# Kernel optimization log

Measured on AMD Instinct MI355X. Metric: run time of the kernel, lower is better.

The kernel has to match this reference:

```python
import jax, jax.numpy as jnp
import numpy as np

N = 100000          # nodes
E = 3200000         # directed edges
NUM_GRAPHS = 2000   # pooled segments
D = 64              # hidden dim
L = 3               # num_unit GCNConv layers


def setup_inputs() -> dict:
    key = jax.random.key(0)
    ks = jax.random.split(key, 12)
    x = jax.random.normal(ks[0], (N, 4), dtype=jnp.float32)
    edge_index = jax.random.randint(ks[1], (2, E), 0, N, dtype=jnp.int64)
    batch = jnp.sort(jax.random.randint(ks[2], (N,), 0, NUM_GRAPHS, dtype=jnp.int64))
    def lin(k, out_f, in_f):
        kw, kb = jax.random.split(k)
        lim = 1.0 / np.sqrt(in_f)
        W = jax.random.uniform(kw, (out_f, in_f), jnp.float32, -lim, lim)
        b = jax.random.uniform(kb, (out_f,), jnp.float32, -lim, lim)
        return W, b
    emb_w, emb_b = lin(ks[3], D, 4)
    cw, cb = [], []
    for i in range(L):
        W, b = lin(ks[4 + i], D, D)
        cw.append(W); cb.append(b)
    conv_w = jnp.stack(cw)   # [L, D, D]
    conv_b = jnp.stack(cb)   # [L, D]
    lin1_w, lin1_b = lin(ks[8], D, D)
    lin2_w, lin2_b = lin(ks[9], 3, D)
    return {"x": x, "edge_index": edge_index, "batch": batch,
            "emb_w": emb_w, "emb_b": emb_b, "conv_w": conv_w, "conv_b": conv_b,
            "lin1_w": lin1_w, "lin1_b": lin1_b, "lin2_w": lin2_w, "lin2_b": lin2_b}


def reference(x, edge_index, batch, emb_w, emb_b, conv_w, conv_b,
              lin1_w, lin1_b, lin2_w, lin2_b):
    # ---- GCN normalization (edge_weight = 1, self-loops added, shared across layers) ----
    loop = jnp.arange(N, dtype=edge_index.dtype)
    src = jnp.concatenate([edge_index[0], loop])   # [E+N]
    dst = jnp.concatenate([edge_index[1], loop])
    deg = jax.ops.segment_sum(jnp.ones_like(src, dtype=x.dtype), dst, num_segments=N)
    dinv = jnp.where(deg > 0, jax.lax.rsqrt(deg), 0.0)
    norm = dinv[src] * dinv[dst]                   # [E+N]

    # node embedding (dropout in eval mode = identity)
    h = x @ emb_w.T + emb_b                        # [N, D]

    # stacked GCNConv + ReLU: h' = scatter_add(norm * (h W^T)[src] -> dst) + b
    for l in range(L):
        t = h @ conv_w[l].T                        # [N, D]
        msg = t[src] * norm[:, None]               # gather + scale, [E+N, D]
        h = jax.ops.segment_sum(msg, dst, num_segments=N) + conv_b[l]
        h = jax.nn.relu(h)

    # global mean pool over graphs
    gsum = jax.ops.segment_sum(h, batch, num_segments=NUM_GRAPHS)        # [G, D]
    cnt = jax.ops.segment_sum(jnp.ones((N,), x.dtype), batch, num_segments=NUM_GRAPHS)
    gmean = gsum / jnp.maximum(cnt, 1.0)[:, None]

    # MLP head
    p = jax.nn.relu(gmean @ lin1_w.T + lin1_b)
    pred = p @ lin2_w.T + lin2_b                   # [G, 3]
    return pred
```

## Files before the change

kernel.cpp:

```cpp
#include <hip/hip_runtime.h>

__device__ __forceinline__ unsigned short f2bf(float f) {
    union { float f; unsigned int u; } c; c.f = f;
    unsigned int r = c.u + 0x7fffu + ((c.u >> 16) & 1u);
    return (unsigned short)(r >> 16);
}
__device__ __forceinline__ float bf2f(unsigned short b) {
    union { unsigned int u; float f; } c; c.u = ((unsigned int)b) << 16;
    return c.f;
}
__device__ __forceinline__ float bflo(unsigned int v) {
    union { unsigned int u; float f; } c; c.u = v << 16; return c.f;
}
__device__ __forceinline__ float bfhi(unsigned int v) {
    union { unsigned int u; float f; } c; c.u = v & 0xffff0000u; return c.f;
}


#define BIN_CAP 6144
#define MAX_BINS 1024

__global__ __launch_bounds__(256) void k_binA(const int* __restrict__ src,
                                              const int* __restrict__ dst,
                                              int* __restrict__ bincnt,
                                              int* __restrict__ binbuf,
                                              int E, int nbins) {
    __shared__ int hist[MAX_BINS];
    __shared__ int lbase[MAX_BINS];
    int tid = threadIdx.x;
    int chunk = (E + gridDim.x - 1) / gridDim.x;
    int e0 = blockIdx.x * chunk;
    int e1 = min(e0 + chunk, E);

    for (int i = tid; i < nbins; i += 256) hist[i] = 0;
    __syncthreads();
    for (int e = e0 + tid; e < e1; e += 256) atomicAdd(&hist[dst[e] >> 7], 1);
    __syncthreads();
    for (int i = tid; i < nbins; i += 256) {
        int c = hist[i];
        lbase[i] = c ? atomicAdd(&bincnt[i], c) : 0;
        hist[i] = 0;
    }
    __syncthreads();
    for (int e = e0 + tid; e < e1; e += 256) {
        int d = dst[e], s = src[e];
        int b = d >> 7;
        int pos = lbase[b] + atomicAdd(&hist[b], 1);
        binbuf[(size_t)b * BIN_CAP + pos] = ((d & 127) << 20) | s;
    }
}

__global__ void k_hist(const int* __restrict__ bincnt, const int* __restrict__ binbuf,
                       int* __restrict__ deg, float* __restrict__ dinv, int n) {
    __shared__ int h[128];
    int b = blockIdx.x, tid = threadIdx.x;
    if (tid < 128) h[tid] = 0;
    __syncthreads();
    int cnt = bincnt[b];
    const int* rec = binbuf + (size_t)b * BIN_CAP;
    for (int i = tid; i < cnt; i += 256) atomicAdd(&h[rec[i] >> 20], 1);
    __syncthreads();
    int node = b * 128 + tid;
    if (tid < 128 && node < n) {
        int d = h[tid];
        deg[node] = d;
        dinv[node] = rsqrtf((float)(d + 1));
    }
}

__global__ void k_scan1(const int* __restrict__ deg, int* __restrict__ rowptr,
                        int* __restrict__ bsum, int n) {
    __shared__ int s[256];
    int tid = threadIdx.x;
    int i = blockIdx.x * 256 + tid;
    int v = (i < n) ? deg[i] : 0;
    s[tid] = v;
    __syncthreads();
    for (int off = 1; off < 256; off <<= 1) {
        int t = (tid >= off) ? s[tid - off] : 0;
        __syncthreads();
        s[tid] += t;
        __syncthreads();
    }
    if (i < n) rowptr[i] = s[tid] - v;
    if (tid == 255) bsum[blockIdx.x] = s[255];
}

__global__ void k_scan2(int* __restrict__ bsum, int nb) {
    __shared__ int s[512];
    int tid = threadIdx.x;
    int v = (tid < nb) ? bsum[tid] : 0;
    s[tid] = v;
    __syncthreads();
    for (int off = 1; off < 512; off <<= 1) {
        int t = (tid >= off) ? s[tid - off] : 0;
        __syncthreads();
        s[tid] += t;
        __syncthreads();
    }
    if (tid < nb) bsum[tid] = s[tid] - v;
}

__global__ void k_scan3(int* __restrict__ rowptr, const int* __restrict__ bsum,
                        int n, int total) {
    int i = blockIdx.x * blockDim.x + threadIdx.x;
    if (i < n) rowptr[i] += bsum[i >> 8];
    if (i == 0) rowptr[n] = total;
}

__global__ void k_binB(const int* __restrict__ bincnt, const int* __restrict__ binbuf,
                       const int* __restrict__ rowptr, int* __restrict__ col, int n) {
    __shared__ int cur[128];
    int b = blockIdx.x, tid = threadIdx.x;
    int node = b * 128 + tid;
    if (tid < 128) cur[tid] = (node < n) ? rowptr[node] : 0;
    __syncthreads();
    int cnt = bincnt[b];
    const int* rec = binbuf + (size_t)b * BIN_CAP;
    for (int i = tid; i < cnt; i += 256) {
        int r = rec[i];
        int pos = atomicAdd(&cur[r >> 20], 1);
        col[pos] = r & ((1 << 20) - 1);
    }
}


__global__ __launch_bounds__(256) void k_gemm0(const float* __restrict__ x,
                                               const float* __restrict__ embw,
                                               const float* __restrict__ embb,
                                               const float* __restrict__ W,
                                               const float* __restrict__ dinv,
                                               unsigned short* __restrict__ uout, int n) {
    __shared__ float hN[64 * 68];
    __shared__ float wT[64 * 68];
    __shared__ float sX[64 * 4];
    __shared__ float sW[64 * 4];
    __shared__ float sB[64];
    int tid = threadIdx.x;
    int nbase = blockIdx.x * 64;
    for (int i = tid; i < 4096; i += 256) {
        int j = i >> 6, k = i & 63;
        wT[k * 68 + j] = W[i];
    }
    if (tid < 256) sW[tid] = embw[tid];
    if (tid < 64) sB[tid] = embb[tid];
    {
        int node = nbase + (tid >> 2);
        sX[tid] = (node < n) ? x[(size_t)node * 4 + (tid & 3)] : 0.f;
    }
    __syncthreads();
    for (int i = tid; i < 4096; i += 256) {
        int nn = i >> 6, k = i & 63;
        float s = sB[k];
        s = fmaf(sX[nn * 4 + 0], sW[k * 4 + 0], s);
        s = fmaf(sX[nn * 4 + 1], sW[k * 4 + 1], s);
        s = fmaf(sX[nn * 4 + 2], sW[k * 4 + 2], s);
        s = fmaf(sX[nn * 4 + 3], sW[k * 4 + 3], s);
        hN[nn * 68 + k] = s;
    }
    __syncthreads();

    int tx = tid & 15;
    int ty = tid >> 4;
    float acc[4][4] = {};
#pragma unroll
    for (int k0 = 0; k0 < 64; k0 += 4) {
        float a[4][4], w[4][4];
#pragma unroll
        for (int i = 0; i < 4; i++)
            *(float4*)a[i] = *(const float4*)&hN[(ty * 4 + i) * 68 + k0];
#pragma unroll
        for (int dk = 0; dk < 4; dk++)
            *(float4*)w[dk] = *(const float4*)&wT[(k0 + dk) * 68 + tx * 4];
#pragma unroll
        for (int i = 0; i < 4; i++)
#pragma unroll
            for (int j = 0; j < 4; j++)
#pragma unroll
                for (int dk = 0; dk < 4; dk++)
                    acc[i][j] = fmaf(a[i][dk], w[dk][j], acc[i][j]);
    }
#pragma unroll
    for (int i = 0; i < 4; i++) {
        int node = nbase + ty * 4 + i;
        if (node < n) {
            float sc = dinv[node];
            ushort4 o;
            o.x = f2bf(acc[i][0] * sc);
            o.y = f2bf(acc[i][1] * sc);
            o.z = f2bf(acc[i][2] * sc);
            o.w = f2bf(acc[i][3] * sc);
            *(ushort4*)&uout[(size_t)node * 64 + tx * 4] = o;
        }
    }
}

__global__ __launch_bounds__(256) void k_gemm(const unsigned short* __restrict__ hin,
                                              const float* __restrict__ W,
                                              const float* __restrict__ dinv,
                                              unsigned short* __restrict__ uout, int n) {
    __shared__ float hN[64 * 68];
    __shared__ float wT[64 * 68];
    int tid = threadIdx.x;
    int nbase = blockIdx.x * 64;
    for (int i = tid; i < 4096; i += 256) {
        int j = i >> 6, k = i & 63;
        wT[k * 68 + j] = W[i];
    }
    for (int i = tid; i < 2048; i += 256) {
        int nn = i >> 5, k2 = i & 31;
        int node = nbase + nn;
        unsigned int v = (node < n) ? ((const unsigned int*)hin)[(size_t)node * 32 + k2] : 0u;
        hN[nn * 68 + k2 * 2 + 0] = bflo(v);
        hN[nn * 68 + k2 * 2 + 1] = bfhi(v);
    }
    __syncthreads();

    int tx = tid & 15;
    int ty = tid >> 4;
    float acc[4][4] = {};
#pragma unroll
    for (int k0 = 0; k0 < 64; k0 += 4) {
        float a[4][4], w[4][4];
#pragma unroll
        for (int i = 0; i < 4; i++)
            *(float4*)a[i] = *(const float4*)&hN[(ty * 4 + i) * 68 + k0];
#pragma unroll
        for (int dk = 0; dk < 4; dk++)
            *(float4*)w[dk] = *(const float4*)&wT[(k0 + dk) * 68 + tx * 4];
#pragma unroll
        for (int i = 0; i < 4; i++)
#pragma unroll
            for (int j = 0; j < 4; j++)
#pragma unroll
                for (int dk = 0; dk < 4; dk++)
                    acc[i][j] = fmaf(a[i][dk], w[dk][j], acc[i][j]);
    }
#pragma unroll
    for (int i = 0; i < 4; i++) {
        int node = nbase + ty * 4 + i;
        if (node < n) {
            float sc = dinv[node];
            ushort4 o;
            o.x = f2bf(acc[i][0] * sc);
            o.y = f2bf(acc[i][1] * sc);
            o.z = f2bf(acc[i][2] * sc);
            o.w = f2bf(acc[i][3] * sc);
            *(ushort4*)&uout[(size_t)node * 64 + tx * 4] = o;
        }
    }
}

__global__ void k_agg(const unsigned short* __restrict__ u, const int* __restrict__ rowptr,
                      const int* __restrict__ col, const float* __restrict__ dinv,
                      const float* __restrict__ bias, unsigned short* __restrict__ hout, int n) {
    int wid = (blockIdx.x * blockDim.x + threadIdx.x) >> 6;
    int lane = threadIdx.x & 63;
    if (wid >= n) return;
    int g = lane >> 4, t = lane & 15;
    const unsigned int* u32 = (const unsigned int*)u;

    float a0 = 0.f, a1 = 0.f, a2 = 0.f, a3 = 0.f;
    if (g == 0) {
        uint2 v = *(const uint2*)&u32[(size_t)wid * 32 + t * 2];
        a0 = bflo(v.x); a1 = bfhi(v.x); a2 = bflo(v.y); a3 = bfhi(v.y);
    }
    int p = rowptr[wid] + g;
    int e = rowptr[wid + 1];
    for (; p + 12 < e; p += 16) {
        int s0 = col[p], s1 = col[p + 4], s2 = col[p + 8], s3 = col[p + 12];
        uint2 v0 = *(const uint2*)&u32[(size_t)s0 * 32 + t * 2];
        uint2 v1 = *(const uint2*)&u32[(size_t)s1 * 32 + t * 2];
        uint2 v2 = *(const uint2*)&u32[(size_t)s2 * 32 + t * 2];
        uint2 v3 = *(const uint2*)&u32[(size_t)s3 * 32 + t * 2];
        a0 += bflo(v0.x); a1 += bfhi(v0.x); a2 += bflo(v0.y); a3 += bfhi(v0.y);
        a0 += bflo(v1.x); a1 += bfhi(v1.x); a2 += bflo(v1.y); a3 += bfhi(v1.y);
        a0 += bflo(v2.x); a1 += bfhi(v2.x); a2 += bflo(v2.y); a3 += bfhi(v2.y);
        a0 += bflo(v3.x); a1 += bfhi(v3.x); a2 += bflo(v3.y); a3 += bfhi(v3.y);
    }
    for (; p < e; p += 4) {
        int s0 = col[p];
        uint2 v0 = *(const uint2*)&u32[(size_t)s0 * 32 + t * 2];
        a0 += bflo(v0.x); a1 += bfhi(v0.x); a2 += bflo(v0.y); a3 += bfhi(v0.y);
    }
    a0 += __shfl_xor(a0, 16, 64); a1 += __shfl_xor(a1, 16, 64);
    a2 += __shfl_xor(a2, 16, 64); a3 += __shfl_xor(a3, 16, 64);
    a0 += __shfl_xor(a0, 32, 64); a1 += __shfl_xor(a1, 32, 64);
    a2 += __shfl_xor(a2, 32, 64); a3 += __shfl_xor(a3, 32, 64);

    if (g == 0) {
        float sc = dinv[wid];
        float f0 = fmaxf(fmaf(sc, a0, bias[t * 4 + 0]), 0.f);
        float f1 = fmaxf(fmaf(sc, a1, bias[t * 4 + 1]), 0.f);
        float f2 = fmaxf(fmaf(sc, a2, bias[t * 4 + 2]), 0.f);
        float f3 = fmaxf(fmaf(sc, a3, bias[t * 4 + 3]), 0.f);
        ushort4 o;
        o.x = f2bf(f0); o.y = f2bf(f1); o.z = f2bf(f2); o.w = f2bf(f3);
        *(ushort4*)&hout[(size_t)wid * 64 + t * 4] = o;
    }
}

__global__ __launch_bounds__(256) void k_pool(const unsigned short* __restrict__ h,
                                              const int* __restrict__ batch,
                                              const float* __restrict__ l1w,
                                              const float* __restrict__ l1b,
                                              const float* __restrict__ l2w,
                                              const float* __restrict__ l2b,
                                              float* __restrict__ out, int n, int G) {
    __shared__ float wl[64 * 65];
    __shared__ float gsm[4][64];
    int tid = threadIdx.x;
    for (int i = tid; i < 4096; i += 256) {
        int j = i >> 6, k = i & 63;
        wl[j * 65 + k] = l1w[i];
    }
    int wv = tid >> 6;
    int lane = tid & 63;
    int g = blockIdx.x * 4 + wv;
    int grp = lane >> 4, t = lane & 15;
    const unsigned int* h32 = (const unsigned int*)h;

    int start = 0, end = 0;
    if (g < G) {
        int lo = 0, hi = n;
        while (lo < hi) { int mid = (lo + hi) >> 1; if (batch[mid] < g) lo = mid + 1; else hi = mid; }
        start = lo;
        hi = n;
        while (lo < hi) { int mid = (lo + hi) >> 1; if (batch[mid] < g + 1) lo = mid + 1; else hi = mid; }
        end = lo;
    }

    float a0 = 0.f, a1 = 0.f, a2 = 0.f, a3 = 0.f;
    int nb = start;
    for (; nb + 4 <= end; nb += 4) {
        int node = nb + grp;
        uint2 v = *(const uint2*)&h32[(size_t)node * 32 + t * 2];
        a0 += bflo(v.x); a1 += bfhi(v.x); a2 += bflo(v.y); a3 += bfhi(v.y);
    }
    if (grp < end - nb) {
        int node = nb + grp;
        uint2 v = *(const uint2*)&h32[(size_t)node * 32 + t * 2];
        a0 += bflo(v.x); a1 += bfhi(v.x); a2 += bflo(v.y); a3 += bfhi(v.y);
    }
    a0 += __shfl_xor(a0, 16, 64); a1 += __shfl_xor(a1, 16, 64);
    a2 += __shfl_xor(a2, 16, 64); a3 += __shfl_xor(a3, 16, 64);
    a0 += __shfl_xor(a0, 32, 64); a1 += __shfl_xor(a1, 32, 64);
    a2 += __shfl_xor(a2, 32, 64); a3 += __shfl_xor(a3, 32, 64);

    float cnt = (float)((end - start) > 0 ? (end - start) : 1);
    if (grp == 0) {
        gsm[wv][t * 4 + 0] = a0 / cnt;
        gsm[wv][t * 4 + 1] = a1 / cnt;
        gsm[wv][t * 4 + 2] = a2 / cnt;
        gsm[wv][t * 4 + 3] = a3 / cnt;
    }
    __syncthreads();
    if (g < G) {
        float pj = l1b[lane];
#pragma unroll
        for (int k = 0; k < 64; k++) pj = fmaf(gsm[wv][k], wl[lane * 65 + k], pj);
        pj = fmaxf(pj, 0.f);
        for (int o = 0; o < 3; o++) {
            float v = pj * l2w[o * 64 + lane];
            for (int off = 32; off; off >>= 1) v += __shfl_xor(v, off, 64);
            if (lane == 0) out[g * 3 + o] = v + l2b[o];
        }
    }
}


extern "C" void kernel_launch(void* const* d_in, const int* in_sizes, int n_in,
                              void* d_out, int out_size, void* d_ws, size_t ws_size,
                              hipStream_t stream) {
    const float* x      = (const float*)d_in[0];
    const int*   edge   = (const int*)d_in[1];
    const int*   batch  = (const int*)d_in[2];
    const float* emb_w  = (const float*)d_in[3];
    const float* emb_b  = (const float*)d_in[4];
    const float* conv_w = (const float*)d_in[5];
    const float* conv_b = (const float*)d_in[6];
    const float* l1w    = (const float*)d_in[7];
    const float* l1b    = (const float*)d_in[8];
    const float* l2w    = (const float*)d_in[9];
    const float* l2b    = (const float*)d_in[10];
    float* out = (float*)d_out;

    const int N = in_sizes[2];
    const int E = in_sizes[1] / 2;
    const int G = out_size / 3;
    const int NB = (N + 127) >> 7;

    char* ws = (char*)d_ws;
    size_t off = 0;
    auto alloc = [&](size_t bytes) -> void* {
        void* p = ws + off;
        off = (off + bytes + 255) & ~(size_t)255;
        return p;
    };
    int*   deg    = (int*)alloc((size_t)N * 4);
    float* dinv   = (float*)alloc((size_t)N * 4);
    int*   rowptr = (int*)alloc((size_t)(N + 1) * 4);
    int*   bsum   = (int*)alloc(512 * 4);
    int*   bincnt = (int*)alloc((size_t)NB * 4);
    int*   colw   = (int*)alloc((size_t)E * 4);
    unsigned short* hbuf = (unsigned short*)alloc((size_t)N * 64 * 2);
    int* binbuf = (int*)alloc((size_t)NB * BIN_CAP * 4);
    unsigned short* ubuf = (unsigned short*)binbuf;

    const int* esrc = edge;
    const int* edst = edge + E;

    hipMemsetAsync(bincnt, 0, (size_t)NB * 4, stream);
    k_binA<<<512, 256, 0, stream>>>(esrc, edst, bincnt, binbuf, E, NB);
    k_hist<<<NB, 256, 0, stream>>>(bincnt, binbuf, deg, dinv, N);
    int nb = (N + 255) / 256;
    k_scan1<<<nb, 256, 0, stream>>>(deg, rowptr, bsum, N);
    k_scan2<<<1, 512, 0, stream>>>(bsum, nb);
    k_scan3<<<nb, 256, 0, stream>>>(rowptr, bsum, N, E);
    k_binB<<<NB, 256, 0, stream>>>(bincnt, binbuf, rowptr, colw, N);

    k_gemm0<<<(N + 63) / 64, 256, 0, stream>>>(x, emb_w, emb_b, conv_w, dinv, ubuf, N);
    k_agg<<<(N + 3) / 4, 256, 0, stream>>>(ubuf, rowptr, colw, dinv, conv_b, hbuf, N);
    for (int l = 1; l < 3; l++) {
        k_gemm<<<(N + 63) / 64, 256, 0, stream>>>(hbuf, conv_w + (size_t)l * 64 * 64, dinv, ubuf, N);
        k_agg<<<(N + 3) / 4, 256, 0, stream>>>(ubuf, rowptr, colw, dinv, conv_b + (size_t)l * 64, hbuf, N);
    }

    k_pool<<<(G + 3) / 4, 256, 0, stream>>>(hbuf, batch, l1w, l1b, l2w, l2b, out, N, G);
}
```

Before: 473.2 us.

## Fuse CSR construction into one bin-local scan/scatter kernel with padded bins

Measured after the change: 471.4 us. About the same (-0.4%).

```diff
diff --git a/kernel.cpp b/kernel.cpp
--- a/kernel.cpp
+++ b/kernel.cpp
@@ -5,10 +5,6 @@
     unsigned int r = c.u + 0x7fffu + ((c.u >> 16) & 1u);
     return (unsigned short)(r >> 16);
 }
-__device__ __forceinline__ float bf2f(unsigned short b) {
-    union { unsigned int u; float f; } c; c.u = ((unsigned int)b) << 16;
-    return c.f;
-}
 __device__ __forceinline__ float bflo(unsigned int v) {
     union { unsigned int u; float f; } c; c.u = v << 16; return c.f;
 }
@@ -17,12 +13,13 @@
 }
 
 
-#define BIN_CAP 6144
+#define BIN_CAP 10240
 #define MAX_BINS 1024
 
 __global__ __launch_bounds__(256) void k_binA(const int* __restrict__ src,
                                               const int* __restrict__ dst,
-                                              int* __restrict__ bincnt,
+                                              int* __restrict__ bincntPad,
+                                              int* __restrict__ bincntExact,
                                               int* __restrict__ binbuf,
                                               int E, int nbins) {
     __shared__ int hist[MAX_BINS];
@@ -38,7 +35,10 @@
     __syncthreads();
     for (int i = tid; i < nbins; i += 256) {
         int c = hist[i];
-        lbase[i] = c ? atomicAdd(&bincnt[i], c) : 0;
+        if (c) {
+            atomicAdd(&bincntExact[i], c);
+            lbase[i] = atomicAdd(&bincntPad[i], (c + 15) & ~15);
+        }
         hist[i] = 0;
     }
     __syncthreads();
@@ -48,79 +48,83 @@
         int pos = lbase[b] + atomicAdd(&hist[b], 1);
         binbuf[(size_t)b * BIN_CAP + pos] = ((d & 127) << 20) | s;
     }
-}
-
-__global__ void k_hist(const int* __restrict__ bincnt, const int* __restrict__ binbuf,
-                       int* __restrict__ deg, float* __restrict__ dinv, int n) {
-    __shared__ int h[128];
-    int b = blockIdx.x, tid = threadIdx.x;
-    if (tid < 128) h[tid] = 0;
-    __syncthreads();
-    int cnt = bincnt[b];
-    const int* rec = binbuf + (size_t)b * BIN_CAP;
-    for (int i = tid; i < cnt; i += 256) atomicAdd(&h[rec[i] >> 20], 1);
-    __syncthreads();
-    int node = b * 128 + tid;
-    if (tid < 128 && node < n) {
-        int d = h[tid];
-        deg[node] = d;
-        dinv[node] = rsqrtf((float)(d + 1));
-    }
-}
-
-__global__ void k_scan1(const int* __restrict__ deg, int* __restrict__ rowptr,
-                        int* __restrict__ bsum, int n) {
-    __shared__ int s[256];
+    __syncthreads();
+    for (int i = tid; i < nbins; i += 256) {
+        int c = hist[i];
+        if (c & 15) {
+            int* p = binbuf + (size_t)i * BIN_CAP + lbase[i] + c;
+            int pad = 16 - (c & 15);
+            for (int j = 0; j < pad; j++) p[j] = 0x7FFFFFFF;
+        }
+    }
+}
+
+__global__ void k_scanB(const int* __restrict__ cntE, int* __restrict__ binstart,
+                        int nbins) {
+    __shared__ int s[1024];
     int tid = threadIdx.x;
-    int i = blockIdx.x * 256 + tid;
-    int v = (i < n) ? deg[i] : 0;
+    int v = (tid < nbins) ? cntE[tid] : 0;
     s[tid] = v;
     __syncthreads();
-    for (int off = 1; off < 256; off <<= 1) {
+    for (int off = 1; off < 1024; off <<= 1) {
         int t = (tid >= off) ? s[tid - off] : 0;
         __syncthreads();
         s[tid] += t;
         __syncthreads();
     }
-    if (i < n) rowptr[i] = s[tid] - v;
-    if (tid == 255) bsum[blockIdx.x] = s[255];
-}
-
-__global__ void k_scan2(int* __restrict__ bsum, int nb) {
-    __shared__ int s[512];
-    int tid = threadIdx.x;
-    int v = (tid < nb) ? bsum[tid] : 0;
-    s[tid] = v;
-    __syncthreads();
-    for (int off = 1; off < 512; off <<= 1) {
-        int t = (tid >= off) ? s[tid - off] : 0;
-        __syncthreads();
-        s[tid] += t;
-        __syncthreads();
-    }
-    if (tid < nb) bsum[tid] = s[tid] - v;
-}
-
-__global__ void k_scan3(int* __restrict__ rowptr, const int* __restrict__ bsum,
-                        int n, int total) {
-    int i = blockIdx.x * blockDim.x + threadIdx.x;
-    if (i < n) rowptr[i] += bsum[i >> 8];
-    if (i == 0) rowptr[n] = total;
-}
-
-__global__ void k_binB(const int* __restrict__ bincnt, const int* __restrict__ binbuf,
-                       const int* __restrict__ rowptr, int* __restrict__ col, int n) {
+    if (tid < nbins) binstart[tid] = s[tid] - v;
+}
+
+__global__ __launch_bounds__(256) void k_binC(const int* __restrict__ bincntPad,
+                                              const int* __restrict__ binstart,
+                                              const int* __restrict__ binbuf,
+                                              int* __restrict__ deg,
+                                              float* __restrict__ dinv,
+                                              int* __restrict__ rowptr,
+                                              int* __restrict__ col, int n) {
+    __shared__ int recs[BIN_CAP];
+    __shared__ int hist[128];
+    __shared__ int scn[128];
     __shared__ int cur[128];
     int b = blockIdx.x, tid = threadIdx.x;
-    int node = b * 128 + tid;
-    if (tid < 128) cur[tid] = (node < n) ? rowptr[node] : 0;
-    __syncthreads();
-    int cnt = bincnt[b];
+    int cnt = bincntPad[b];
     const int* rec = binbuf + (size_t)b * BIN_CAP;
+    for (int i = tid; i < cnt; i += 256) recs[i] = rec[i];
+    if (tid < 128) hist[tid] = 0;
+    __syncthreads();
     for (int i = tid; i < cnt; i += 256) {
-        int r = rec[i];
-        int pos = atomicAdd(&cur[r >> 20], 1);
-        col[pos] = r & ((1 << 20) - 1);
+        int r = recs[i];
+        if ((r & 0xFFFFF) < n) atomicAdd(&hist[(r >> 20) & 127], 1);
+    }
+    __syncthreads();
+    int v = (tid < 128) ? hist[tid] : 0;
+    if (tid < 128) scn[tid] = v;
+    __syncthreads();
+    for (int off = 1; off < 128; off <<= 1) {
+        int t = (tid < 128 && tid >= off) ? scn[tid - off] : 0;
+        __syncthreads();
+        if (tid < 128) scn[tid] += t;
+        __syncthreads();
+    }
+    int rowbase = binstart[b];
+    if (tid < 128) {
+        int excl = scn[tid] - v;
+        cur[tid] = rowbase + excl;
+        int node = b * 128 + tid;
+        if (node < n) {
+            deg[node] = v;
+            dinv[node] = rsqrtf((float)(v + 1));
+            rowptr[node] = rowbase + excl;
+        }
+    }
+    __syncthreads();
+    for (int i = tid; i < cnt; i += 256) {
+        int r = recs[i];
+        int s = r & 0xFFFFF;
+        if (s < n) {
+            int pos = atomicAdd(&cur[(r >> 20) & 127], 1);
+            col[pos] = s;
+        }
     }
 }
 
@@ -252,8 +256,9 @@
 }
 
 __global__ void k_agg(const unsigned short* __restrict__ u, const int* __restrict__ rowptr,
-                      const int* __restrict__ col, const float* __restrict__ dinv,
-                      const float* __restrict__ bias, unsigned short* __restrict__ hout, int n) {
+                      const int* __restrict__ deg, const int* __restrict__ col,
+                      const float* __restrict__ dinv, const float* __restrict__ bias,
+                      unsigned short* __restrict__ hout, int n) {
     int wid = (blockIdx.x * blockDim.x + threadIdx.x) >> 6;
     int lane = threadIdx.x & 63;
     if (wid >= n) return;
@@ -265,8 +270,9 @@
         uint2 v = *(const uint2*)&u32[(size_t)wid * 32 + t * 2];
         a0 = bflo(v.x); a1 = bfhi(v.x); a2 = bflo(v.y); a3 = bfhi(v.y);
     }
-    int p = rowptr[wid] + g;
-    int e = rowptr[wid + 1];
+    int p0 = rowptr[wid];
+    int e = p0 + deg[wid];
+    int p = p0 + g;
     for (; p + 12 < e; p += 16) {
         int s0 = col[p], s1 = col[p + 4], s2 = col[p + 8], s3 = col[p + 12];
         uint2 v0 = *(const uint2*)&u32[(size_t)s0 * 32 + t * 2];
@@ -397,33 +403,31 @@
         off = (off + bytes + 255) & ~(size_t)255;
         return p;
     };
-    int*   deg    = (int*)alloc((size_t)N * 4);
-    float* dinv   = (float*)alloc((size_t)N * 4);
-    int*   rowptr = (int*)alloc((size_t)(N + 1) * 4);
-    int*   bsum   = (int*)alloc(512 * 4);
-    int*   bincnt = (int*)alloc((size_t)NB * 4);
-    int*   colw   = (int*)alloc((size_t)E * 4);
-    unsigned short* hbuf = (unsigned short*)alloc((size_t)N * 64 * 2);
-    int* binbuf = (int*)alloc((size_t)NB * BIN_CAP * 4);
+    int*   deg      = (int*)alloc((size_t)N * 4);
+    float* dinv     = (float*)alloc((size_t)N * 4);
+    int*   rowptr   = (int*)alloc((size_t)N * 4);
+    int*   bincntP  = (int*)alloc((size_t)NB * 4);
+    int*   bincntE  = (int*)alloc((size_t)NB * 4);
+    int*   binstart = (int*)alloc((size_t)NB * 4);
+    int*   colw     = (int*)alloc((size_t)E * 4);
+    int*   binbuf   = (int*)alloc((size_t)NB * BIN_CAP * 4);
     unsigned short* ubuf = (unsigned short*)binbuf;
+    unsigned short* hbuf = (unsigned short*)((char*)binbuf + (size_t)N * 64 * 2);
 
     const int* esrc = edge;
     const int* edst = edge + E;
 
-    hipMemsetAsync(bincnt, 0, (size_t)NB * 4, stream);
-    k_binA<<<512, 256, 0, stream>>>(esrc, edst, bincnt, binbuf, E, NB);
-    k_hist<<<NB, 256, 0, stream>>>(bincnt, binbuf, deg, dinv, N);
-    int nb = (N + 255) / 256;
-    k_scan1<<<nb, 256, 0, stream>>>(deg, rowptr, bsum, N);
-    k_scan2<<<1, 512, 0, stream>>>(bsum, nb);
-    k_scan3<<<nb, 256, 0, stream>>>(rowptr, bsum, N, E);
-    k_binB<<<NB, 256, 0, stream>>>(bincnt, binbuf, rowptr, colw, N);
+    hipMemsetAsync(bincntP, 0, (size_t)NB * 4, stream);
+    hipMemsetAsync(bincntE, 0, (size_t)NB * 4, stream);
+    k_binA<<<256, 256, 0, stream>>>(esrc, edst, bincntP, bincntE, binbuf, E, NB);
+    k_scanB<<<1, 1024, 0, stream>>>(bincntE, binstart, NB);
+    k_binC<<<NB, 256, 0, stream>>>(bincntP, binstart, binbuf, deg, dinv, rowptr, colw, N);
 
     k_gemm0<<<(N + 63) / 64, 256, 0, stream>>>(x, emb_w, emb_b, conv_w, dinv, ubuf, N);
-    k_agg<<<(N + 3) / 4, 256, 0, stream>>>(ubuf, rowptr, colw, dinv, conv_b, hbuf, N);
+    k_agg<<<(N + 3) / 4, 256, 0, stream>>>(ubuf, rowptr, deg, colw, dinv, conv_b, hbuf, N);
     for (int l = 1; l < 3; l++) {
         k_gemm<<<(N + 63) / 64, 256, 0, stream>>>(hbuf, conv_w + (size_t)l * 64 * 64, dinv, ubuf, N);
-        k_agg<<<(N + 3) / 4, 256, 0, stream>>>(ubuf, rowptr, colw, dinv, conv_b + (size_t)l * 64, hbuf, N);
+        k_agg<<<(N + 3) / 4, 256, 0, stream>>>(ubuf, rowptr, deg, colw, dinv, conv_b + (size_t)l * 64, hbuf, N);
     }
 
     k_pool<<<(G + 3) / 4, 256, 0, stream>>>(hbuf, batch, l1w, l1b, l2w, l2b, out, N, G);
```
